# Kernel tuning notes

Measured on AMD Instinct MI355X. Metric: run time of the kernel, lower is better.

Reference implementation:

```python
import jax, jax.numpy as jnp
import numpy as np

B, N, CA, CS, CZ, H, NQ, NK = 2, 16384, 128, 128, 16, 4, 32, 128
DH = CA // H
NB = N // NQ


def _ln(x, gamma=None, eps=1e-5):
    m = jnp.mean(x, -1, keepdims=True)
    v = jnp.var(x, -1, keepdims=True)
    y = (x - m) * jax.lax.rsqrt(v + eps)
    return y if gamma is None else y * gamma


def _adaln(a, s, gamma_s, Wg, bg, Wskip):
    # AF3 Algorithm 26: LN(a) without affine; LN(s) with scale, no offset;
    # out = sigmoid(Linear(s)) * a + LinearNoBias(s)
    a_n = _ln(a)
    s_n = _ln(s, gamma_s)
    return jax.nn.sigmoid(s_n @ Wg + bg) * a_n + s_n @ Wskip


def setup_inputs():
    key = jax.random.key(0)
    ks = jax.random.split(key, 20)
    def nrm(i, shape, scale=0.02):
        return jax.random.normal(ks[i], shape, jnp.float32) * scale
    return {
        "a": jax.random.normal(ks[0], (B, N, CA), jnp.float32),
        "s": jax.random.normal(ks[1], (B, N, CS), jnp.float32),
        "z": jax.random.normal(ks[2], (B, NB, NQ, NK, CZ), jnp.float32),
        "apb_gamma_s": jnp.ones((CS,), jnp.float32),
        "apb_Wg": nrm(3, (CS, CA)),
        "apb_bg": jnp.zeros((CA,), jnp.float32),
        "apb_Wskip": nrm(4, (CS, CA)),
        "Wq": nrm(5, (CA, CA)), "bq": jnp.zeros((CA,), jnp.float32),
        "Wk": nrm(6, (CA, CA)), "Wv": nrm(7, (CA, CA)),
        "Wgate": nrm(8, (CA, CA)), "Wo": nrm(9, (CA, CA)),
        "gamma_z": jnp.ones((CZ,), jnp.float32),
        "Wz": nrm(10, (CZ, H)),
        "Ws_last": nrm(11, (CS, CA)),
        "bs_last": jnp.full((CA,), -2.0, jnp.float32),
        "ct_gamma_s": jnp.ones((CS,), jnp.float32),
        "ct_Wg": nrm(12, (CS, CA)), "ct_bg": jnp.zeros((CA,), jnp.float32),
        "ct_Wskip": nrm(13, (CS, CA)),
        "Wa1": nrm(14, (CA, 2 * CA)), "Wa2": nrm(15, (CA, 2 * CA)),
        "Wb": nrm(16, (2 * CA, CA)),
        "Ws": nrm(17, (CS, CA)), "bs": jnp.full((CA,), -2.0, jnp.float32),
        "n_queries": NQ, "n_keys": NK,
    }


def reference(a, s, z, apb_gamma_s, apb_Wg, apb_bg, apb_Wskip, Wq, bq, Wk, Wv,
              Wgate, Wo, gamma_z, Wz, Ws_last, bs_last, ct_gamma_s, ct_Wg,
              ct_bg, ct_Wskip, Wa1, Wa2, Wb, Ws, bs, n_queries, n_keys):
    nq, nk = int(n_queries), int(n_keys)
    nb = N // nq
    # ---- AttentionPairBias, local windowed attention ----
    a1 = _adaln(a, s, apb_gamma_s, apb_Wg, apb_bg, apb_Wskip)  # [B,N,CA]
    # trunked pair bias: [B,nb,nq,nk,H] -> [B,H,nb,nq,nk]
    bias = jnp.transpose(_ln(z, gamma_z) @ Wz, (0, 4, 1, 2, 3))
    q = (a1 @ Wq + bq).reshape(B, N, H, DH).transpose(0, 2, 1, 3)
    k = (a1 @ Wk).reshape(B, N, H, DH).transpose(0, 2, 1, 3)
    v = (a1 @ Wv).reshape(B, N, H, DH).transpose(0, 2, 1, 3)
    qb = q.reshape(B, H, nb, nq, DH)
    pad = (nk - nq) // 2
    # centered key window per query block
    idx = (jnp.arange(nb) * nq - pad)[:, None] + jnp.arange(nk)[None, :]  # [nb,nk]
    valid = (idx >= 0) & (idx < N)
    idxc = jnp.clip(idx, 0, N - 1)
    kb = k[:, :, idxc]  # [B,H,nb,nk,DH]
    vb = v[:, :, idxc]
    scores = jnp.einsum('bhnqd,bhnkd->bhnqk', qb, kb) / np.sqrt(DH).astype(np.float32) + bias
    scores = jnp.where(valid[None, None, :, None, :], scores, -1e9)
    attn = jax.nn.softmax(scores, axis=-1)
    o = jnp.einsum('bhnqk,bhnkd->bhnqd', attn, vb)  # [B,H,nb,nq,DH]
    o = o.reshape(B, H, N, DH).transpose(0, 2, 1, 3).reshape(B, N, CA)
    g = jax.nn.sigmoid(a1 @ Wgate)  # per-channel gating
    attn_out = (g * o) @ Wo
    b_out = jax.nn.sigmoid(s @ Ws_last + bs_last) * attn_out
    # ---- ConditionedTransitionBlock (Alg 25) ----
    a3 = _adaln(a, s, ct_gamma_s, ct_Wg, ct_bg, ct_Wskip)
    t = jax.nn.silu(a3 @ Wa1) * (a3 @ Wa2)
    ct_out = jax.nn.sigmoid(s @ Ws + bs) * (t @ Wb)
    # Alg 23: a = b + ConditionedTransitionBlock(a, s)
    return b_out + ct_out
```

## Files before the change

kernel.cpp:

```cpp
#include <hip/hip_runtime.h>

typedef _Float16 f16;
typedef f16 f16x8 __attribute__((ext_vector_type(8)));
typedef f16 f16x4 __attribute__((ext_vector_type(4)));
typedef f16 f16x2 __attribute__((ext_vector_type(2)));
typedef float f32x4 __attribute__((ext_vector_type(4)));

#define MFMA16(a,b,c) __builtin_amdgcn_mfma_f32_16x16x32_f16((a),(b),(c),0,0,0)

static __device__ __forceinline__ f16x8 ld8(const f16* p){ return *(const f16x8*)p; }
static __device__ __forceinline__ float sigm(float x){ return 1.f/(1.f + __expf(-x)); }

__global__ __launch_bounds__(256) void k_prep(
    const float* __restrict__ apb_gamma, const float* __restrict__ apb_Wg, const float* __restrict__ apb_Wskip,
    const float* __restrict__ ct_gamma,  const float* __restrict__ ct_Wg,  const float* __restrict__ ct_Wskip,
    const float* __restrict__ Wq, const float* __restrict__ Wk, const float* __restrict__ Wv, const float* __restrict__ Wgate,
    const float* __restrict__ Wsl, const float* __restrict__ Wss,
    const float* __restrict__ Wa1, const float* __restrict__ Wa2,
    const float* __restrict__ Wo, const float* __restrict__ Wb,
    const float* __restrict__ gamma_z, const float* __restrict__ Wz,
    f16* __restrict__ wA, f16* __restrict__ wC, f16* __restrict__ wQK, f16* __restrict__ wVG,
    f16* __restrict__ wSG, f16* __restrict__ wAB, f16* __restrict__ wO, f16* __restrict__ wBt,
    float* __restrict__ wzg, float* __restrict__ Slv, float* __restrict__ Ssv)
{
  const int t0 = blockIdx.x*256 + threadIdx.x;
  const int stride = gridDim.x*256;
  for (int i = t0; i < 256*128; i += stride){
    const int n = i >> 7, k = i & 127;
    const int m = n & 127;
    wA[i]  = (f16)(((n<128) ? apb_Wg[k*128+m] : apb_Wskip[k*128+m]) * apb_gamma[k]);
    wC[i]  = (f16)(((n<128) ? ct_Wg[k*128+m]  : ct_Wskip[k*128+m])  * ct_gamma[k]);
    wQK[i] = (f16)((n<128) ? Wq[k*128+m] : Wk[k*128+m]);
    wVG[i] = (f16)((n<128) ? Wv[k*128+m] : Wgate[k*128+m]);
    wSG[i] = (f16)((n<128) ? Wsl[k*128+m] : Wss[k*128+m]);
  }
  for (int i = t0; i < 512*128; i += stride){
    const int n = i >> 7, k = i & 127;
    wAB[i] = (f16)((n < 256) ? Wa1[k*256 + n] : Wa2[k*256 + (n-256)]);
  }
  for (int i = t0; i < 128*128; i += stride){
    const int n = i >> 7, k = i & 127;
    wO[i] = (f16)Wo[k*128+n];
  }
  for (int i = t0; i < 128*256; i += stride){
    const int n = i >> 8, k = i & 255;
    wBt[i] = (f16)Wb[k*128+n];
  }
  if (t0 < 64) wzg[t0] = gamma_z[t0 & 15] * Wz[(t0 & 15)*4 + (t0 >> 4)];
  if (t0 < 256){
    const int cc = t0 & 127;
    const float* Wp = (t0 >= 128) ? Wss : Wsl;
    float acc = 0.f;
    for (int k = 0; k < 128; k++) acc += Wp[k*128 + cc];
    if (t0 >= 128) Ssv[cc] = acc; else Slv[cc] = acc;
  }
}

__global__ __launch_bounds__(256) void k_pre(
    const float* __restrict__ A, const float* __restrict__ S,
    const f16* __restrict__ wA, const f16* __restrict__ wC,
    const f16* __restrict__ wQK, const f16* __restrict__ wVG,
    const f16* __restrict__ wSG, const f16* __restrict__ wAB,
    const float* __restrict__ bgA, const float* __restrict__ bgC,
    const float* __restrict__ bq, const float* __restrict__ bsl, const float* __restrict__ bss,
    const float* __restrict__ Slv, const float* __restrict__ Ssv,
    f16* __restrict__ Qo, f16* __restrict__ Ko, f16* __restrict__ Vt, f16* __restrict__ Go,
    f16* __restrict__ T, f16* __restrict__ GL, f16* __restrict__ GS)
{
  __shared__ f16 lsn[64*136];
  __shared__ f16 lan[64*136];
  __shared__ f16 la1[64*136];
  __shared__ f16 la3[64*136];
  __shared__ float lsm[64], lsd[64];
  const int tid = threadIdx.x;
  const size_t rbase = (size_t)blockIdx.x * 64;

  {
    const int row = tid >> 2, part = tid & 3;
    const size_t gr = rbase + row;
    {
      const float* sp = S + gr*128 + part*32;
      float v[32];
      #pragma unroll
      for (int j = 0; j < 8; j++){
        const float4 t4 = ((const float4*)sp)[j];
        v[j*4+0]=t4.x; v[j*4+1]=t4.y; v[j*4+2]=t4.z; v[j*4+3]=t4.w;
      }
      float sm = 0.f, sq = 0.f;
      #pragma unroll
      for (int j = 0; j < 32; j++){ sm += v[j]; sq += v[j]*v[j]; }
      sm += __shfl_xor(sm,1); sq += __shfl_xor(sq,1);
      sm += __shfl_xor(sm,2); sq += __shfl_xor(sq,2);
      const float mean = sm*(1.f/128.f);
      const float var  = sq*(1.f/128.f) - mean*mean;
      const float rstd = rsqrtf(var + 1e-5f);
      if (part == 0){ lsm[row] = mean; lsd[row] = (var + 1e-5f)*rstd; }
      #pragma unroll
      for (int j = 0; j < 4; j++){
        f16x8 o;
        #pragma unroll
        for (int e = 0; e < 8; e++) o[e] = (f16)((v[j*8+e]-mean)*rstd);
        *(f16x8*)&lsn[row*136 + part*32 + j*8] = o;
      }
    }
    {
      const float* ap = A + gr*128 + part*32;
      float v[32];
      #pragma unroll
      for (int j = 0; j < 8; j++){
        const float4 t4 = ((const float4*)ap)[j];
        v[j*4+0]=t4.x; v[j*4+1]=t4.y; v[j*4+2]=t4.z; v[j*4+3]=t4.w;
      }
      float sm = 0.f, sq = 0.f;
      #pragma unroll
      for (int j = 0; j < 32; j++){ sm += v[j]; sq += v[j]*v[j]; }
      sm += __shfl_xor(sm,1); sq += __shfl_xor(sq,1);
      sm += __shfl_xor(sm,2); sq += __shfl_xor(sq,2);
      const float mean = sm*(1.f/128.f);
      const float var  = sq*(1.f/128.f) - mean*mean;
      const float rstd = rsqrtf(var + 1e-5f);
      #pragma unroll
      for (int j = 0; j < 4; j++){
        f16x8 o;
        #pragma unroll
        for (int e = 0; e < 8; e++) o[e] = (f16)((v[j*8+e]-mean)*rstd);
        *(f16x8*)&lan[row*136 + part*32 + j*8] = o;
      }
    }
  }
  __syncthreads();

  const int l = tid & 63, w = tid >> 6;
  const int c = l & 15, q4 = l >> 4;

  for (int jj = 0; jj < 4; jj++){
    const int job = jj*4 + w;
    const int n0 = (job >> 1)*16;
    const int mat = job & 1;
    const f16* W = mat ? wC : wA;
    f16* dst = mat ? la3 : la1;
    const float bv = (mat ? bgC : bgA)[n0 + c];
    f16x8 b0[4], b1[4];
    #pragma unroll
    for (int kc = 0; kc < 4; kc++){
      b0[kc] = ld8(W + (size_t)(n0 + c)*128 + kc*32 + q4*8);
      b1[kc] = ld8(W + (size_t)(128 + n0 + c)*128 + kc*32 + q4*8);
    }
    for (int mi = 0; mi < 4; mi++){
      f32x4 d0 = {0,0,0,0}, d1 = {0,0,0,0};
      #pragma unroll
      for (int kc = 0; kc < 4; kc++){
        const f16x8 av = *(const f16x8*)&lsn[(mi*16 + c)*136 + kc*32 + q4*8];
        d0 = MFMA16(av, b0[kc], d0);
        d1 = MFMA16(av, b1[kc], d1);
      }
      #pragma unroll
      for (int r = 0; r < 4; r++){
        const int row = mi*16 + q4*4 + r;
        const float anv = (float)lan[row*136 + n0 + c];
        dst[row*136 + n0 + c] = (f16)(sigm(d0[r] + bv)*anv + d1[r]);
      }
    }
  }
  __syncthreads();

  for (int jj = 0; jj < 2; jj++){
    const int n0 = (jj*4 + w)*16;
    f16x8 bQ[4], bK[4], bV[4], bG[4];
    #pragma unroll
    for (int kc = 0; kc < 4; kc++){
      bQ[kc] = ld8(wQK + (size_t)(n0 + c)*128 + kc*32 + q4*8);
      bK[kc] = ld8(wQK + (size_t)(128 + n0 + c)*128 + kc*32 + q4*8);
      bV[kc] = ld8(wVG + (size_t)(n0 + c)*128 + kc*32 + q4*8);
      bG[kc] = ld8(wVG + (size_t)(128 + n0 + c)*128 + kc*32 + q4*8);
    }
    const float bvq = bq[n0 + c];
    for (int mi = 0; mi < 4; mi++){
      f32x4 dQ = {0,0,0,0}, dK = {0,0,0,0}, dV = {0,0,0,0}, dG = {0,0,0,0};
      #pragma unroll
      for (int kc = 0; kc < 4; kc++){
        const f16x8 av = *(const f16x8*)&la1[(mi*16 + c)*136 + kc*32 + q4*8];
        dQ = MFMA16(av, bQ[kc], dQ);
        dK = MFMA16(av, bK[kc], dK);
        dV = MFMA16(av, bV[kc], dV);
        dG = MFMA16(av, bG[kc], dG);
      }
      #pragma unroll
      for (int r = 0; r < 4; r++){
        const size_t grow = rbase + mi*16 + q4*4 + r;
        Qo[grow*128 + n0 + c] = (f16)((dQ[r] + bvq)*0.17677669529663687f);
        Ko[grow*128 + n0 + c] = (f16)dK[r];
        Go[grow*128 + n0 + c] = (f16)sigm(dG[r]);
      }
      f16x4 vv;
      #pragma unroll
      for (int r = 0; r < 4; r++) vv[r] = (f16)dV[r];
      const int bidx = (int)(rbase >> 14);
      const int ntk  = (int)(rbase & 16383) + mi*16 + q4*4;
      *(f16x4*)(Vt + ((size_t)bidx*128 + n0 + c)*16384 + ntk) = vv;
    }
  }

  for (int jj = 0; jj < 4; jj++){
    const int n0t = (jj*4 + w)*16;
    f16x8 b1v[4], b2v[4];
    #pragma unroll
    for (int kc = 0; kc < 4; kc++){
      b1v[kc] = ld8(wAB + (size_t)(n0t + c)*128 + kc*32 + q4*8);
      b2v[kc] = ld8(wAB + (size_t)(256 + n0t + c)*128 + kc*32 + q4*8);
    }
    for (int mi = 0; mi < 4; mi++){
      f32x4 d0 = {0,0,0,0}, d1 = {0,0,0,0};
      #pragma unroll
      for (int kc = 0; kc < 4; kc++){
        const f16x8 av = *(const f16x8*)&la3[(mi*16 + c)*136 + kc*32 + q4*8];
        d0 = MFMA16(av, b1v[kc], d0);
        d1 = MFMA16(av, b2v[kc], d1);
      }
      #pragma unroll
      for (int r = 0; r < 4; r++){
        const size_t grow = rbase + mi*16 + q4*4 + r;
        const float u = d0[r];
        T[grow*256 + n0t + c] = (f16)((u*sigm(u))*d1[r]);
      }
    }
  }

  for (int jj = 0; jj < 2; jj++){
    const int n0 = (jj*4 + w)*16;
    f16x8 b0[4], b1[4];
    #pragma unroll
    for (int kc = 0; kc < 4; kc++){
      b0[kc] = ld8(wSG + (size_t)(n0 + c)*128 + kc*32 + q4*8);
      b1[kc] = ld8(wSG + (size_t)(128 + n0 + c)*128 + kc*32 + q4*8);
    }
    const float slc = Slv[n0 + c], ssc = Ssv[n0 + c];
    const float bl = bsl[n0 + c],  bs2 = bss[n0 + c];
    for (int mi = 0; mi < 4; mi++){
      f32x4 d0 = {0,0,0,0}, d1 = {0,0,0,0};
      #pragma unroll
      for (int kc = 0; kc < 4; kc++){
        const f16x8 av = *(const f16x8*)&lsn[(mi*16 + c)*136 + kc*32 + q4*8];
        d0 = MFMA16(av, b0[kc], d0);
        d1 = MFMA16(av, b1[kc], d1);
      }
      #pragma unroll
      for (int r = 0; r < 4; r++){
        const int row = mi*16 + q4*4 + r;
        const size_t grow = rbase + row;
        const float mn = lsm[row], sd = lsd[row];
        GL[grow*128 + n0 + c] = (f16)sigm(d0[r]*sd + mn*slc + bl);
        GS[grow*128 + n0 + c] = (f16)sigm(d1[r]*sd + mn*ssc + bs2);
      }
    }
  }
}

__global__ __launch_bounds__(512) void k_attn(const f16* __restrict__ Q, const f16* __restrict__ K,
    const f16* __restrict__ VT, const float* __restrict__ Z, const float* __restrict__ WZG,
    f16* __restrict__ Og)
{
  __shared__ f16 upb[17408];
  __shared__ float wzg_s[64];
  const int tid = threadIdx.x;
  const int b = blockIdx.x >> 9, nb = blockIdx.x & 511;
  if (tid < 64) wzg_s[tid] = WZG[tid];
  __syncthreads();
  #pragma unroll
  for (int i = 0; i < 8; i++){
    const int p  = tid + i*512;
    const int qq = p >> 7, kk = p & 127;
    const float* zp = Z + ((((size_t)b*512 + nb)*32 + qq)*128 + kk)*16;
    const float4 z0 = *(const float4*)(zp);
    const float4 z1 = *(const float4*)(zp + 4);
    const float4 z2 = *(const float4*)(zp + 8);
    const float4 z3 = *(const float4*)(zp + 12);
    const float xs[16] = {z0.x,z0.y,z0.z,z0.w, z1.x,z1.y,z1.z,z1.w,
                          z2.x,z2.y,z2.z,z2.w, z3.x,z3.y,z3.z,z3.w};
    float sm = 0.f, sq = 0.f;
    #pragma unroll
    for (int cc = 0; cc < 16; cc++){ sm += xs[cc]; sq += xs[cc]*xs[cc]; }
    const float mean = sm*(1.f/16.f);
    const float var  = sq*(1.f/16.f) - mean*mean;
    const float rs   = rsqrtf(var + 1e-5f);
    #pragma unroll
    for (int h = 0; h < 4; h++){
      float acc = 0.f;
      #pragma unroll
      for (int cc = 0; cc < 16; cc++) acc += (xs[cc]-mean)*wzg_s[h*16+cc];
      upb[(h*32 + qq)*132 + kk] = (f16)(acc*rs);
    }
  }
  __syncthreads();

  const int l = tid & 63, w = tid >> 6;
  const int c = l & 15, q4 = l >> 4;
  const int h = w >> 1, qh = w & 1, m0 = qh*16;
  const f16x8 aq = ld8(Q + ((size_t)b*16384 + (size_t)nb*32 + m0 + c)*128 + h*32 + q4*8);
  const long kbase = (long)b*16384 + (long)nb*32 - 48;
  f32x4 sc[8];
  #pragma unroll
  for (int nt = 0; nt < 8; nt++){
    const f16x8 bf = ld8(K + (kbase + nt*16 + c)*128 + h*32 + q4*8);
    f32x4 zz = {0.f,0.f,0.f,0.f};
    sc[nt] = MFMA16(aq, bf, zz);
  }
  #pragma unroll
  for (int nt = 0; nt < 8; nt++){
    const int key = nt*16 + c;
    const long kt = (long)nb*32 - 48 + key;
    const bool inv = (kt < 0) || (kt >= 16384);
    #pragma unroll
    for (int r = 0; r < 4; r++){
      const float v = sc[nt][r] + (float)upb[(h*32 + m0 + q4*4 + r)*132 + key];
      sc[nt][r] = inv ? -1e9f : v;
    }
  }
  #pragma unroll
  for (int r = 0; r < 4; r++){
    float mx = sc[0][r];
    #pragma unroll
    for (int nt = 1; nt < 8; nt++) mx = fmaxf(mx, sc[nt][r]);
    #pragma unroll
    for (int o = 8; o; o >>= 1) mx = fmaxf(mx, __shfl_xor(mx, o));
    float sum = 0.f;
    #pragma unroll
    for (int nt = 0; nt < 8; nt++){ const float e = __expf(sc[nt][r]-mx); sc[nt][r] = e; sum += e; }
    #pragma unroll
    for (int o = 8; o; o >>= 1) sum += __shfl_xor(sum, o);
    const float inv = 1.f/sum;
    #pragma unroll
    for (int nt = 0; nt < 8; nt++) sc[nt][r] *= inv;
  }
  __syncthreads();
  #pragma unroll
  for (int nt = 0; nt < 8; nt++)
    #pragma unroll
    for (int r = 0; r < 4; r++)
      upb[(w*16 + q4*4 + r)*136 + nt*16 + c] = (f16)sc[nt][r];
  const f16* vb = VT + ((long)b*128)*16384 + (long)nb*32 - 48;
  f32x4 o0 = {0.f,0.f,0.f,0.f}, o1 = {0.f,0.f,0.f,0.f};
  #pragma unroll
  for (int kc = 0; kc < 4; kc++){
    const f16x8 pa = *(const f16x8*)&upb[(w*16 + c)*136 + kc*32 + q4*8];
    const f16x8 v0 = ld8(vb + (long)(h*32 + c)*16384 + kc*32 + q4*8);
    const f16x8 v1 = ld8(vb + (long)(h*32 + 16 + c)*16384 + kc*32 + q4*8);
    o0 = MFMA16(pa, v0, o0);
    o1 = MFMA16(pa, v1, o1);
  }
  #pragma unroll
  for (int r = 0; r < 4; r++){
    const size_t tok = (size_t)b*16384 + (size_t)nb*32 + m0 + q4*4 + r;
    Og[tok*128 + h*32 + c]      = (f16)o0[r];
    Og[tok*128 + h*32 + 16 + c] = (f16)o1[r];
  }
}

__global__ __launch_bounds__(256) void k_final(const f16* __restrict__ G, const f16* __restrict__ O,
    const f16* __restrict__ T, const f16* __restrict__ Wot, const f16* __restrict__ Wbt,
    const f16* __restrict__ GL, const f16* __restrict__ GS, float* __restrict__ out)
{
  const int l = threadIdx.x & 63, w = threadIdx.x >> 6;
  const int c = l & 15, q4 = l >> 4;
  const int mbase = blockIdx.x*64 + w*16;
  f16x8 ag[4], at[8];
  const f16* gp = G + (size_t)(mbase + c)*128 + q4*8;
  const f16* op = O + (size_t)(mbase + c)*128 + q4*8;
  #pragma unroll
  for (int kc = 0; kc < 4; kc++) ag[kc] = ld8(gp + kc*32) * ld8(op + kc*32);
  const f16* tp = T + (size_t)(mbase + c)*256 + q4*8;
  #pragma unroll
  for (int kc = 0; kc < 8; kc++) at[kc] = ld8(tp + kc*32);
  for (int nt = 0; nt < 8; nt++){
    const int cb = nt*16;
    f32x4 d1 = {0,0,0,0}, d2 = {0,0,0,0};
    #pragma unroll
    for (int kc = 0; kc < 4; kc++)
      d1 = MFMA16(ag[kc], ld8(Wot + (size_t)(cb + c)*128 + kc*32 + q4*8), d1);
    #pragma unroll
    for (int kc = 0; kc < 8; kc++)
      d2 = MFMA16(at[kc], ld8(Wbt + (size_t)(cb + c)*256 + kc*32 + q4*8), d2);
    #pragma unroll
    for (int r = 0; r < 4; r++){
      const size_t row = mbase + q4*4 + r;
      const float glv = (float)GL[row*128 + cb + c];
      const float gsv = (float)GS[row*128 + cb + c];
      out[row*128 + cb + c] = glv*d1[r] + gsv*d2[r];
    }
  }
}

extern "C" void kernel_launch(void* const* d_in, const int* in_sizes, int n_in,
                              void* d_out, int out_size, void* d_ws, size_t ws_size,
                              hipStream_t stream)
{
  (void)in_sizes; (void)n_in; (void)out_size; (void)ws_size;
  const float* a        = (const float*)d_in[0];
  const float* s        = (const float*)d_in[1];
  const float* z        = (const float*)d_in[2];
  const float* apb_gamma= (const float*)d_in[3];
  const float* apb_Wg   = (const float*)d_in[4];
  const float* apb_bg   = (const float*)d_in[5];
  const float* apb_Wskip= (const float*)d_in[6];
  const float* Wq       = (const float*)d_in[7];
  const float* bq       = (const float*)d_in[8];
  const float* Wk       = (const float*)d_in[9];
  const float* Wv       = (const float*)d_in[10];
  const float* Wgate    = (const float*)d_in[11];
  const float* Wo       = (const float*)d_in[12];
  const float* gamma_z  = (const float*)d_in[13];
  const float* Wz       = (const float*)d_in[14];
  const float* Wsl      = (const float*)d_in[15];
  const float* bsl      = (const float*)d_in[16];
  const float* ct_gamma = (const float*)d_in[17];
  const float* ct_Wg    = (const float*)d_in[18];
  const float* ct_bg    = (const float*)d_in[19];
  const float* ct_Wskip = (const float*)d_in[20];
  const float* Wa1      = (const float*)d_in[21];
  const float* Wa2      = (const float*)d_in[22];
  const float* Wb       = (const float*)d_in[23];
  const float* Wss      = (const float*)d_in[24];
  const float* bss      = (const float*)d_in[25];

  f16* W0 = (f16*)d_ws;
  const size_t SL = (size_t)32768*128;
  f16* qv = W0 + 0*SL;
  f16* kv = W0 + 1*SL;
  f16* vt = W0 + 2*SL;
  f16* gv = W0 + 3*SL;
  f16* tv = W0 + 4*SL;
  f16* gl = W0 + 6*SL;
  f16* gs = W0 + 7*SL;
  f16* ov = W0 + 8*SL;
  f16* wA  = W0 + 9*SL;
  f16* wC  = wA  + 256*128;
  f16* wQK = wC  + 256*128;
  f16* wVG = wQK + 256*128;
  f16* wSG = wVG + 256*128;
  f16* wAB = wSG + 256*128;
  f16* wO  = wAB + 512*128;
  f16* wBt = wO  + 128*128;
  float* wzg = (float*)(wBt + 128*256);
  float* Slv = wzg + 64;
  float* Ssv = Slv + 128;

  k_prep<<<dim3(64),256,0,stream>>>(apb_gamma,apb_Wg,apb_Wskip, ct_gamma,ct_Wg,ct_Wskip,
      Wq,Wk,Wv,Wgate, Wsl,Wss, Wa1,Wa2, Wo,Wb, gamma_z,Wz,
      wA,wC,wQK,wVG,wSG,wAB,wO,wBt,wzg,Slv,Ssv);
  k_pre<<<dim3(512),256,0,stream>>>(a,s, wA,wC,wQK,wVG,wSG,wAB,
      apb_bg,ct_bg,bq,bsl,bss,Slv,Ssv, qv,kv,vt,gv,tv,gl,gs);
  k_attn<<<dim3(1024),512,0,stream>>>(qv,kv,vt,z,wzg,ov);
  k_final<<<dim3(512),256,0,stream>>>(gv,ov,tv,wO,wBt,gl,gs,(float*)d_out);
}
```

Baseline: 534.1 us.

## Halve row tiles, swap MFMA operands for vectorized stores, reuse LDS

k_pre and k_final now process 32 rows per block instead of 64 and launch twice as many blocks. k_pre drops the la3 buffer by writing a3 into lan, and loads the S and A LayerNorms on separate halves of the block. Most MFMAs now take the weight as the first operand, so each lane holds four consecutive output columns and can write f16x4/float4 vectors instead of scalar stores. The attention softmax is rearranged to match the transposed score layout, with cross-lane reductions over lanes 16 and 32. The aim is higher occupancy and better-coalesced stores, at the cost of reloading weights in twice as many blocks.

```diff
diff --git a/kernel.cpp b/kernel.cpp
--- a/kernel.cpp
+++ b/kernel.cpp
@@ -3,7 +3,6 @@
 typedef _Float16 f16;
 typedef f16 f16x8 __attribute__((ext_vector_type(8)));
 typedef f16 f16x4 __attribute__((ext_vector_type(4)));
-typedef f16 f16x2 __attribute__((ext_vector_type(2)));
 typedef float f32x4 __attribute__((ext_vector_type(4)));
 
 #define MFMA16(a,b,c) __builtin_amdgcn_mfma_f32_16x16x32_f16((a),(b),(c),0,0,0)
@@ -56,7 +55,7 @@
   }
 }
 
-__global__ __launch_bounds__(256) void k_pre(
+__global__ __launch_bounds__(256, 4) void k_pre(
     const float* __restrict__ A, const float* __restrict__ S,
     const f16* __restrict__ wA, const f16* __restrict__ wC,
     const f16* __restrict__ wQK, const f16* __restrict__ wVG,
@@ -67,65 +66,40 @@
     f16* __restrict__ Qo, f16* __restrict__ Ko, f16* __restrict__ Vt, f16* __restrict__ Go,
     f16* __restrict__ T, f16* __restrict__ GL, f16* __restrict__ GS)
 {
-  __shared__ f16 lsn[64*136];
-  __shared__ f16 lan[64*136];
-  __shared__ f16 la1[64*136];
-  __shared__ f16 la3[64*136];
-  __shared__ float lsm[64], lsd[64];
+  __shared__ f16 lsn[32*136];
+  __shared__ f16 lan[32*136];
+  __shared__ f16 la1[32*136];
+  __shared__ float lsm[32], lsd[32];
   const int tid = threadIdx.x;
-  const size_t rbase = (size_t)blockIdx.x * 64;
+  const size_t rbase = (size_t)blockIdx.x * 32;
 
   {
-    const int row = tid >> 2, part = tid & 3;
+    const int half = tid >> 7;
+    const int row = (tid & 127) >> 2, part = tid & 3;
     const size_t gr = rbase + row;
-    {
-      const float* sp = S + gr*128 + part*32;
-      float v[32];
-      #pragma unroll
-      for (int j = 0; j < 8; j++){
-        const float4 t4 = ((const float4*)sp)[j];
-        v[j*4+0]=t4.x; v[j*4+1]=t4.y; v[j*4+2]=t4.z; v[j*4+3]=t4.w;
-      }
-      float sm = 0.f, sq = 0.f;
-      #pragma unroll
-      for (int j = 0; j < 32; j++){ sm += v[j]; sq += v[j]*v[j]; }
-      sm += __shfl_xor(sm,1); sq += __shfl_xor(sq,1);
-      sm += __shfl_xor(sm,2); sq += __shfl_xor(sq,2);
-      const float mean = sm*(1.f/128.f);
-      const float var  = sq*(1.f/128.f) - mean*mean;
-      const float rstd = rsqrtf(var + 1e-5f);
-      if (part == 0){ lsm[row] = mean; lsd[row] = (var + 1e-5f)*rstd; }
-      #pragma unroll
-      for (int j = 0; j < 4; j++){
-        f16x8 o;
-        #pragma unroll
-        for (int e = 0; e < 8; e++) o[e] = (f16)((v[j*8+e]-mean)*rstd);
-        *(f16x8*)&lsn[row*136 + part*32 + j*8] = o;
-      }
-    }
-    {
-      const float* ap = A + gr*128 + part*32;
-      float v[32];
-      #pragma unroll
-      for (int j = 0; j < 8; j++){
-        const float4 t4 = ((const float4*)ap)[j];
-        v[j*4+0]=t4.x; v[j*4+1]=t4.y; v[j*4+2]=t4.z; v[j*4+3]=t4.w;
-      }
-      float sm = 0.f, sq = 0.f;
-      #pragma unroll
-      for (int j = 0; j < 32; j++){ sm += v[j]; sq += v[j]*v[j]; }
-      sm += __shfl_xor(sm,1); sq += __shfl_xor(sq,1);
-      sm += __shfl_xor(sm,2); sq += __shfl_xor(sq,2);
-      const float mean = sm*(1.f/128.f);
-      const float var  = sq*(1.f/128.f) - mean*mean;
-      const float rstd = rsqrtf(var + 1e-5f);
-      #pragma unroll
-      for (int j = 0; j < 4; j++){
-        f16x8 o;
-        #pragma unroll
-        for (int e = 0; e < 8; e++) o[e] = (f16)((v[j*8+e]-mean)*rstd);
-        *(f16x8*)&lan[row*136 + part*32 + j*8] = o;
-      }
+    const float* p = (half ? A : S) + gr*128 + part*32;
+    float v[32];
+    #pragma unroll
+    for (int j = 0; j < 8; j++){
+      const float4 t4 = ((const float4*)p)[j];
+      v[j*4+0]=t4.x; v[j*4+1]=t4.y; v[j*4+2]=t4.z; v[j*4+3]=t4.w;
+    }
+    float sm = 0.f, sq = 0.f;
+    #pragma unroll
+    for (int j = 0; j < 32; j++){ sm += v[j]; sq += v[j]*v[j]; }
+    sm += __shfl_xor(sm,1); sq += __shfl_xor(sq,1);
+    sm += __shfl_xor(sm,2); sq += __shfl_xor(sq,2);
+    const float mean = sm*(1.f/128.f);
+    const float var  = sq*(1.f/128.f) - mean*mean;
+    const float rstd = rsqrtf(var + 1e-5f);
+    if (!half && part == 0){ lsm[row] = mean; lsd[row] = (var + 1e-5f)*rstd; }
+    f16* dst = half ? lan : lsn;
+    #pragma unroll
+    for (int j = 0; j < 4; j++){
+      f16x8 o;
+      #pragma unroll
+      for (int e = 0; e < 8; e++) o[e] = (f16)((v[j*8+e]-mean)*rstd);
+      *(f16x8*)&dst[row*136 + part*32 + j*8] = o;
     }
   }
   __syncthreads();
@@ -133,74 +107,107 @@
   const int l = tid & 63, w = tid >> 6;
   const int c = l & 15, q4 = l >> 4;
 
-  for (int jj = 0; jj < 4; jj++){
-    const int job = jj*4 + w;
-    const int n0 = (job >> 1)*16;
-    const int mat = job & 1;
-    const f16* W = mat ? wC : wA;
-    f16* dst = mat ? la3 : la1;
-    const float bv = (mat ? bgC : bgA)[n0 + c];
-    f16x8 b0[4], b1[4];
-    #pragma unroll
-    for (int kc = 0; kc < 4; kc++){
-      b0[kc] = ld8(W + (size_t)(n0 + c)*128 + kc*32 + q4*8);
-      b1[kc] = ld8(W + (size_t)(128 + n0 + c)*128 + kc*32 + q4*8);
-    }
-    for (int mi = 0; mi < 4; mi++){
-      f32x4 d0 = {0,0,0,0}, d1 = {0,0,0,0};
-      #pragma unroll
-      for (int kc = 0; kc < 4; kc++){
-        const f16x8 av = *(const f16x8*)&lsn[(mi*16 + c)*136 + kc*32 + q4*8];
-        d0 = MFMA16(av, b0[kc], d0);
-        d1 = MFMA16(av, b1[kc], d1);
-      }
-      #pragma unroll
-      for (int r = 0; r < 4; r++){
-        const int row = mi*16 + q4*4 + r;
-        const float anv = (float)lan[row*136 + n0 + c];
-        dst[row*136 + n0 + c] = (f16)(sigm(d0[r] + bv)*anv + d1[r]);
-      }
-    }
-  }
-  __syncthreads();
-
+  #pragma unroll
   for (int jj = 0; jj < 2; jj++){
     const int n0 = (jj*4 + w)*16;
-    f16x8 bQ[4], bK[4], bV[4], bG[4];
-    #pragma unroll
-    for (int kc = 0; kc < 4; kc++){
-      bQ[kc] = ld8(wQK + (size_t)(n0 + c)*128 + kc*32 + q4*8);
-      bK[kc] = ld8(wQK + (size_t)(128 + n0 + c)*128 + kc*32 + q4*8);
-      bV[kc] = ld8(wVG + (size_t)(n0 + c)*128 + kc*32 + q4*8);
-      bG[kc] = ld8(wVG + (size_t)(128 + n0 + c)*128 + kc*32 + q4*8);
-    }
-    const float bvq = bq[n0 + c];
-    for (int mi = 0; mi < 4; mi++){
-      f32x4 dQ = {0,0,0,0}, dK = {0,0,0,0}, dV = {0,0,0,0}, dG = {0,0,0,0};
+    #pragma unroll
+    for (int mat = 0; mat < 2; mat++){
+      const f16* W = mat ? wC : wA;
+      f16x8 b0[4], b1[4];
       #pragma unroll
       for (int kc = 0; kc < 4; kc++){
-        const f16x8 av = *(const f16x8*)&la1[(mi*16 + c)*136 + kc*32 + q4*8];
-        dQ = MFMA16(av, bQ[kc], dQ);
-        dK = MFMA16(av, bK[kc], dK);
-        dV = MFMA16(av, bV[kc], dV);
-        dG = MFMA16(av, bG[kc], dG);
-      }
-      #pragma unroll
-      for (int r = 0; r < 4; r++){
-        const size_t grow = rbase + mi*16 + q4*4 + r;
-        Qo[grow*128 + n0 + c] = (f16)((dQ[r] + bvq)*0.17677669529663687f);
-        Ko[grow*128 + n0 + c] = (f16)dK[r];
-        Go[grow*128 + n0 + c] = (f16)sigm(dG[r]);
-      }
-      f16x4 vv;
-      #pragma unroll
-      for (int r = 0; r < 4; r++) vv[r] = (f16)dV[r];
-      const int bidx = (int)(rbase >> 14);
-      const int ntk  = (int)(rbase & 16383) + mi*16 + q4*4;
-      *(f16x4*)(Vt + ((size_t)bidx*128 + n0 + c)*16384 + ntk) = vv;
-    }
-  }
-
+        b0[kc] = ld8(W + (size_t)(n0 + c)*128 + kc*32 + q4*8);
+        b1[kc] = ld8(W + (size_t)(128 + n0 + c)*128 + kc*32 + q4*8);
+      }
+      const float4 bv = *(const float4*)((mat ? bgC : bgA) + n0 + q4*4);
+      const float bvr[4] = {bv.x, bv.y, bv.z, bv.w};
+      f16* dst = mat ? lan : la1;
+      #pragma unroll
+      for (int mi = 0; mi < 2; mi++){
+        f32x4 d0 = {0,0,0,0}, d1 = {0,0,0,0};
+        #pragma unroll
+        for (int kc = 0; kc < 4; kc++){
+          const f16x8 av = *(const f16x8*)&lsn[(mi*16 + c)*136 + kc*32 + q4*8];
+          d0 = MFMA16(b0[kc], av, d0);
+          d1 = MFMA16(b1[kc], av, d1);
+        }
+        const int row = mi*16 + c;
+        const f16x4 anv = *(const f16x4*)&lan[row*136 + n0 + q4*4];
+        f16x4 o;
+        #pragma unroll
+        for (int r = 0; r < 4; r++)
+          o[r] = (f16)(sigm(d0[r] + bvr[r])*(float)anv[r] + d1[r]);
+        *(f16x4*)&dst[row*136 + n0 + q4*4] = o;
+      }
+    }
+  }
+  __syncthreads();
+
+  const int bidx = (int)(rbase >> 14);
+  const int ntk0 = (int)(rbase & 16383);
+
+  #pragma unroll
+  for (int jj = 0; jj < 2; jj++){
+    const int n0 = (jj*4 + w)*16;
+    {
+      f16x8 bQ[4], bK[4];
+      #pragma unroll
+      for (int kc = 0; kc < 4; kc++){
+        bQ[kc] = ld8(wQK + (size_t)(n0 + c)*128 + kc*32 + q4*8);
+        bK[kc] = ld8(wQK + (size_t)(128 + n0 + c)*128 + kc*32 + q4*8);
+      }
+      const float4 bv = *(const float4*)(bq + n0 + q4*4);
+      const float bvr[4] = {bv.x, bv.y, bv.z, bv.w};
+      #pragma unroll
+      for (int mi = 0; mi < 2; mi++){
+        f32x4 dQ = {0,0,0,0}, dK = {0,0,0,0};
+        #pragma unroll
+        for (int kc = 0; kc < 4; kc++){
+          const f16x8 av = *(const f16x8*)&la1[(mi*16 + c)*136 + kc*32 + q4*8];
+          dQ = MFMA16(bQ[kc], av, dQ);
+          dK = MFMA16(bK[kc], av, dK);
+        }
+        const size_t grow = rbase + mi*16 + c;
+        f16x4 qo, ko;
+        #pragma unroll
+        for (int r = 0; r < 4; r++){
+          qo[r] = (f16)((dQ[r] + bvr[r])*0.17677669529663687f);
+          ko[r] = (f16)dK[r];
+        }
+        *(f16x4*)&Qo[grow*128 + n0 + q4*4] = qo;
+        *(f16x4*)&Ko[grow*128 + n0 + q4*4] = ko;
+      }
+    }
+    {
+      f16x8 bV[4], bG[4];
+      #pragma unroll
+      for (int kc = 0; kc < 4; kc++){
+        bV[kc] = ld8(wVG + (size_t)(n0 + c)*128 + kc*32 + q4*8);
+        bG[kc] = ld8(wVG + (size_t)(128 + n0 + c)*128 + kc*32 + q4*8);
+      }
+      #pragma unroll
+      for (int mi = 0; mi < 2; mi++){
+        f32x4 dV = {0,0,0,0}, dG = {0,0,0,0};
+        #pragma unroll
+        for (int kc = 0; kc < 4; kc++){
+          const f16x8 av = *(const f16x8*)&la1[(mi*16 + c)*136 + kc*32 + q4*8];
+          dV = MFMA16(av, bV[kc], dV);
+          dG = MFMA16(bG[kc], av, dG);
+        }
+        const size_t grow = rbase + mi*16 + c;
+        f16x4 go;
+        #pragma unroll
+        for (int r = 0; r < 4; r++) go[r] = (f16)sigm(dG[r]);
+        *(f16x4*)&Go[grow*128 + n0 + q4*4] = go;
+        f16x4 vv;
+        #pragma unroll
+        for (int r = 0; r < 4; r++) vv[r] = (f16)dV[r];
+        *(f16x4*)(Vt + ((size_t)bidx*128 + n0 + c)*16384 + ntk0 + mi*16 + q4*4) = vv;
+      }
+    }
+  }
+
+  #pragma unroll
   for (int jj = 0; jj < 4; jj++){
     const int n0t = (jj*4 + w)*16;
     f16x8 b1v[4], b2v[4];
@@ -209,23 +216,27 @@
       b1v[kc] = ld8(wAB + (size_t)(n0t + c)*128 + kc*32 + q4*8);
       b2v[kc] = ld8(wAB + (size_t)(256 + n0t + c)*128 + kc*32 + q4*8);
     }
-    for (int mi = 0; mi < 4; mi++){
+    #pragma unroll
+    for (int mi = 0; mi < 2; mi++){
       f32x4 d0 = {0,0,0,0}, d1 = {0,0,0,0};
       #pragma unroll
       for (int kc = 0; kc < 4; kc++){
-        const f16x8 av = *(const f16x8*)&la3[(mi*16 + c)*136 + kc*32 + q4*8];
-        d0 = MFMA16(av, b1v[kc], d0);
-        d1 = MFMA16(av, b2v[kc], d1);
-      }
+        const f16x8 av = *(const f16x8*)&lan[(mi*16 + c)*136 + kc*32 + q4*8];
+        d0 = MFMA16(b1v[kc], av, d0);
+        d1 = MFMA16(b2v[kc], av, d1);
+      }
+      const size_t grow = rbase + mi*16 + c;
+      f16x4 t4;
       #pragma unroll
       for (int r = 0; r < 4; r++){
-        const size_t grow = rbase + mi*16 + q4*4 + r;
         const float u = d0[r];
-        T[grow*256 + n0t + c] = (f16)((u*sigm(u))*d1[r]);
-      }
-    }
-  }
-
+        t4[r] = (f16)((u*sigm(u))*d1[r]);
+      }
+      *(f16x4*)&T[grow*256 + n0t + q4*4] = t4;
+    }
+  }
+
+  #pragma unroll
   for (int jj = 0; jj < 2; jj++){
     const int n0 = (jj*4 + w)*16;
     f16x8 b0[4], b1[4];
@@ -234,24 +245,34 @@
       b0[kc] = ld8(wSG + (size_t)(n0 + c)*128 + kc*32 + q4*8);
       b1[kc] = ld8(wSG + (size_t)(128 + n0 + c)*128 + kc*32 + q4*8);
     }
-    const float slc = Slv[n0 + c], ssc = Ssv[n0 + c];
-    const float bl = bsl[n0 + c],  bs2 = bss[n0 + c];
-    for (int mi = 0; mi < 4; mi++){
+    const float4 sl4 = *(const float4*)(Slv + n0 + q4*4);
+    const float4 ss4 = *(const float4*)(Ssv + n0 + q4*4);
+    const float4 bl4 = *(const float4*)(bsl + n0 + q4*4);
+    const float4 bs4 = *(const float4*)(bss + n0 + q4*4);
+    const float slr[4] = {sl4.x,sl4.y,sl4.z,sl4.w};
+    const float ssr[4] = {ss4.x,ss4.y,ss4.z,ss4.w};
+    const float blr[4] = {bl4.x,bl4.y,bl4.z,bl4.w};
+    const float bsr[4] = {bs4.x,bs4.y,bs4.z,bs4.w};
+    #pragma unroll
+    for (int mi = 0; mi < 2; mi++){
       f32x4 d0 = {0,0,0,0}, d1 = {0,0,0,0};
       #pragma unroll
       for (int kc = 0; kc < 4; kc++){
         const f16x8 av = *(const f16x8*)&lsn[(mi*16 + c)*136 + kc*32 + q4*8];
-        d0 = MFMA16(av, b0[kc], d0);
-        d1 = MFMA16(av, b1[kc], d1);
-      }
+        d0 = MFMA16(b0[kc], av, d0);
+        d1 = MFMA16(b1[kc], av, d1);
+      }
+      const int row = mi*16 + c;
+      const size_t grow = rbase + row;
+      const float mn = lsm[row], sd = lsd[row];
+      f16x4 gl4, gs4;
       #pragma unroll
       for (int r = 0; r < 4; r++){
-        const int row = mi*16 + q4*4 + r;
-        const size_t grow = rbase + row;
-        const float mn = lsm[row], sd = lsd[row];
-        GL[grow*128 + n0 + c] = (f16)sigm(d0[r]*sd + mn*slc + bl);
-        GS[grow*128 + n0 + c] = (f16)sigm(d1[r]*sd + mn*ssc + bs2);
-      }
+        gl4[r] = (f16)sigm(d0[r]*sd + mn*slr[r] + blr[r]);
+        gs4[r] = (f16)sigm(d1[r]*sd + mn*ssr[r] + bsr[r]);
+      }
+      *(f16x4*)&GL[grow*128 + n0 + q4*4] = gl4;
+      *(f16x4*)&GS[grow*128 + n0 + q4*4] = gs4;
     }
   }
 }
@@ -296,48 +317,48 @@
   const int l = tid & 63, w = tid >> 6;
   const int c = l & 15, q4 = l >> 4;
   const int h = w >> 1, qh = w & 1, m0 = qh*16;
-  const f16x8 aq = ld8(Q + ((size_t)b*16384 + (size_t)nb*32 + m0 + c)*128 + h*32 + q4*8);
+  const f16x8 qf = ld8(Q + ((size_t)b*16384 + (size_t)nb*32 + m0 + c)*128 + h*32 + q4*8);
   const long kbase = (long)b*16384 + (long)nb*32 - 48;
   f32x4 sc[8];
   #pragma unroll
   for (int nt = 0; nt < 8; nt++){
-    const f16x8 bf = ld8(K + (kbase + nt*16 + c)*128 + h*32 + q4*8);
+    const f16x8 kf = ld8(K + (kbase + nt*16 + c)*128 + h*32 + q4*8);
     f32x4 zz = {0.f,0.f,0.f,0.f};
-    sc[nt] = MFMA16(aq, bf, zz);
+    sc[nt] = MFMA16(kf, qf, zz);
   }
   #pragma unroll
   for (int nt = 0; nt < 8; nt++){
-    const int key = nt*16 + c;
-    const long kt = (long)nb*32 - 48 + key;
-    const bool inv = (kt < 0) || (kt >= 16384);
+    const f16x4 bb = *(const f16x4*)&upb[(h*32 + m0 + c)*132 + nt*16 + q4*4];
     #pragma unroll
     for (int r = 0; r < 4; r++){
-      const float v = sc[nt][r] + (float)upb[(h*32 + m0 + q4*4 + r)*132 + key];
-      sc[nt][r] = inv ? -1e9f : v;
-    }
-  }
-  #pragma unroll
-  for (int r = 0; r < 4; r++){
-    float mx = sc[0][r];
-    #pragma unroll
-    for (int nt = 1; nt < 8; nt++) mx = fmaxf(mx, sc[nt][r]);
-    #pragma unroll
-    for (int o = 8; o; o >>= 1) mx = fmaxf(mx, __shfl_xor(mx, o));
-    float sum = 0.f;
-    #pragma unroll
-    for (int nt = 0; nt < 8; nt++){ const float e = __expf(sc[nt][r]-mx); sc[nt][r] = e; sum += e; }
-    #pragma unroll
-    for (int o = 8; o; o >>= 1) sum += __shfl_xor(sum, o);
-    const float inv = 1.f/sum;
-    #pragma unroll
-    for (int nt = 0; nt < 8; nt++) sc[nt][r] *= inv;
-  }
+      const long kt = (long)nb*32 - 48 + nt*16 + q4*4 + r;
+      const bool inv = (kt < 0) || (kt >= 16384);
+      sc[nt][r] = inv ? -1e9f : (sc[nt][r] + (float)bb[r]);
+    }
+  }
+  float mx = sc[0][0];
+  #pragma unroll
+  for (int nt = 0; nt < 8; nt++)
+    #pragma unroll
+    for (int r = 0; r < 4; r++) mx = fmaxf(mx, sc[nt][r]);
+  mx = fmaxf(mx, __shfl_xor(mx, 16));
+  mx = fmaxf(mx, __shfl_xor(mx, 32));
+  float sum = 0.f;
+  #pragma unroll
+  for (int nt = 0; nt < 8; nt++)
+    #pragma unroll
+    for (int r = 0; r < 4; r++){ const float e = __expf(sc[nt][r]-mx); sc[nt][r] = e; sum += e; }
+  sum += __shfl_xor(sum, 16);
+  sum += __shfl_xor(sum, 32);
+  const float inv = 1.f/sum;
   __syncthreads();
   #pragma unroll
-  for (int nt = 0; nt < 8; nt++)
-    #pragma unroll
-    for (int r = 0; r < 4; r++)
-      upb[(w*16 + q4*4 + r)*136 + nt*16 + c] = (f16)sc[nt][r];
+  for (int nt = 0; nt < 8; nt++){
+    f16x4 p4;
+    #pragma unroll
+    for (int r = 0; r < 4; r++) p4[r] = (f16)(sc[nt][r]*inv);
+    *(f16x4*)&upb[(w*16 + c)*136 + nt*16 + q4*4] = p4;
+  }
   const f16* vb = VT + ((long)b*128)*16384 + (long)nb*32 - 48;
   f32x4 o0 = {0.f,0.f,0.f,0.f}, o1 = {0.f,0.f,0.f,0.f};
   #pragma unroll
@@ -356,37 +377,40 @@
   }
 }
 
-__global__ __launch_bounds__(256) void k_final(const f16* __restrict__ G, const f16* __restrict__ O,
+__global__ __launch_bounds__(256, 4) void k_final(const f16* __restrict__ G, const f16* __restrict__ O,
     const f16* __restrict__ T, const f16* __restrict__ Wot, const f16* __restrict__ Wbt,
     const f16* __restrict__ GL, const f16* __restrict__ GS, float* __restrict__ out)
 {
   const int l = threadIdx.x & 63, w = threadIdx.x >> 6;
   const int c = l & 15, q4 = l >> 4;
-  const int mbase = blockIdx.x*64 + w*16;
+  const int rh = w & 1, ch = w >> 1;
+  const size_t mrow = (size_t)blockIdx.x*32 + rh*16 + c;
   f16x8 ag[4], at[8];
-  const f16* gp = G + (size_t)(mbase + c)*128 + q4*8;
-  const f16* op = O + (size_t)(mbase + c)*128 + q4*8;
+  const f16* gp = G + mrow*128 + q4*8;
+  const f16* op = O + mrow*128 + q4*8;
   #pragma unroll
   for (int kc = 0; kc < 4; kc++) ag[kc] = ld8(gp + kc*32) * ld8(op + kc*32);
-  const f16* tp = T + (size_t)(mbase + c)*256 + q4*8;
+  const f16* tp = T + mrow*256 + q4*8;
   #pragma unroll
   for (int kc = 0; kc < 8; kc++) at[kc] = ld8(tp + kc*32);
-  for (int nt = 0; nt < 8; nt++){
-    const int cb = nt*16;
+  #pragma unroll
+  for (int ntl = 0; ntl < 4; ntl++){
+    const int cb = (ch*4 + ntl)*16;
     f32x4 d1 = {0,0,0,0}, d2 = {0,0,0,0};
     #pragma unroll
     for (int kc = 0; kc < 4; kc++)
-      d1 = MFMA16(ag[kc], ld8(Wot + (size_t)(cb + c)*128 + kc*32 + q4*8), d1);
+      d1 = MFMA16(ld8(Wot + (size_t)(cb + c)*128 + kc*32 + q4*8), ag[kc], d1);
     #pragma unroll
     for (int kc = 0; kc < 8; kc++)
-      d2 = MFMA16(at[kc], ld8(Wbt + (size_t)(cb + c)*256 + kc*32 + q4*8), d2);
-    #pragma unroll
-    for (int r = 0; r < 4; r++){
-      const size_t row = mbase + q4*4 + r;
-      const float glv = (float)GL[row*128 + cb + c];
-      const float gsv = (float)GS[row*128 + cb + c];
-      out[row*128 + cb + c] = glv*d1[r] + gsv*d2[r];
-    }
+      d2 = MFMA16(ld8(Wbt + (size_t)(cb + c)*256 + kc*32 + q4*8), at[kc], d2);
+    const f16x4 glv = *(const f16x4*)&GL[mrow*128 + cb + q4*4];
+    const f16x4 gsv = *(const f16x4*)&GS[mrow*128 + cb + q4*4];
+    float4 o;
+    o.x = (float)glv[0]*d1[0] + (float)gsv[0]*d2[0];
+    o.y = (float)glv[1]*d1[1] + (float)gsv[1]*d2[1];
+    o.z = (float)glv[2]*d1[2] + (float)gsv[2]*d2[2];
+    o.w = (float)glv[3]*d1[3] + (float)gsv[3]*d2[3];
+    *(float4*)&out[mrow*128 + cb + q4*4] = o;
   }
 }
 
@@ -447,8 +471,8 @@
   k_prep<<<dim3(64),256,0,stream>>>(apb_gamma,apb_Wg,apb_Wskip, ct_gamma,ct_Wg,ct_Wskip,
       Wq,Wk,Wv,Wgate, Wsl,Wss, Wa1,Wa2, Wo,Wb, gamma_z,Wz,
       wA,wC,wQK,wVG,wSG,wAB,wO,wBt,wzg,Slv,Ssv);
-  k_pre<<<dim3(512),256,0,stream>>>(a,s, wA,wC,wQK,wVG,wSG,wAB,
+  k_pre<<<dim3(1024),256,0,stream>>>(a,s, wA,wC,wQK,wVG,wSG,wAB,
       apb_bg,ct_bg,bq,bsl,bss,Slv,Ssv, qv,kv,vt,gv,tv,gl,gs);
   k_attn<<<dim3(1024),512,0,stream>>>(qv,kv,vt,z,wzg,ov);
-  k_final<<<dim3(512),256,0,stream>>>(gv,ov,tv,wO,wBt,gl,gs,(float*)d_out);
+  k_final<<<dim3(1024),256,0,stream>>>(gv,ov,tv,wO,wBt,gl,gs,(float*)d_out);
 }
```

Measured after the change: 555.9 us. 1.04x slower.
